# Optimization experiments

Hardware: AMD Instinct MI355X
Metric: run time of the kernel (lower is better)

Reference implementation:

```python
import jax, jax.numpy as jnp
import numpy as np

N_NODES = 50000
N_EDGES = 800000
F_IN, HID, N_CLS = 128, 64, 40
KS = 2  # kernel_size, dim=1, open B-spline, degree=1


def spline_conv(x, src, dst, pseudo, W, root, bias, num_nodes, kernel_size):
    """SplineConv (torch_geometric), dim=1, degree=1, open spline, aggr='mean'."""
    K = kernel_size
    v = pseudo[:, 0] * (K - 1)                       # map [0,1] -> [0, K-1]
    k0 = jnp.clip(jnp.floor(v), 0, K - 2)
    frac = v - k0                                    # linear (degree-1) basis
    i0 = k0.astype(jnp.int32)
    i1 = i0 + 1
    E = src.shape[0]
    e = jnp.arange(E)
    # per-edge kernel coefficients c[e,k] = sum_s basis[e,s]*[idx[e,s]==k]
    c = jnp.zeros((E, K), x.dtype).at[e, i0].add(1.0 - frac).at[e, i1].add(frac)
    xj = x[src]                                      # [E, F_in] gather
    # agg[k] = scatter-add over edges of c[e,k]*xj[e] -> [K, N, F_in]
    agg = jnp.stack([
        jax.ops.segment_sum(c[:, k:k + 1] * xj, dst, num_segments=num_nodes)
        for k in range(K)
    ])
    deg = jax.ops.segment_sum(jnp.ones((E,), x.dtype), dst, num_segments=num_nodes)
    msg = jnp.einsum('kni,kio->no', agg, W) / jnp.maximum(deg, 1.0)[:, None]
    return msg + x @ root + bias


def setup_inputs() -> dict:
    key = jax.random.key(0)
    ks = jax.random.split(key, 9)
    def glorot(k, shape):
        fan_in, fan_out = shape[-2], shape[-1]
        lim = (6.0 / (fan_in + fan_out)) ** 0.5
        return jax.random.uniform(k, shape, jnp.float32, -lim, lim)
    return {
        'x': jax.random.normal(ks[0], (N_NODES, F_IN), jnp.float32),
        'edge_index': jax.random.randint(ks[1], (2, N_EDGES), 0, N_NODES, jnp.int32),
        'edge_attr': jax.random.uniform(ks[2], (N_EDGES, 1), jnp.float32),
        'W1': glorot(ks[3], (KS, F_IN, HID)),
        'root1': glorot(ks[4], (F_IN, HID)),
        'bias1': jnp.zeros((HID,), jnp.float32),
        'W2': glorot(ks[5], (KS, HID, N_CLS)),
        'root2': glorot(ks[6], (HID, N_CLS)),
        'bias2': jnp.zeros((N_CLS,), jnp.float32),
    }


def reference(x, edge_index, edge_attr, W1, root1, bias1, W2, root2, bias2):
    src, dst = edge_index[0], edge_index[1]
    # eval mode: dropout is identity
    h = spline_conv(x, src, dst, edge_attr, W1, root1, bias1, N_NODES, KS)
    h = jax.nn.elu(h)
    out = spline_conv(h, src, dst, edge_attr, W2, root2, bias2, N_NODES, KS)
    return out
```

## Files before the change

### kernel.cpp

```cpp
#include <hip/hip_runtime.h>
#include <math.h>

#define N_NODES 50000
#define N_EDGES 800000
#define F_IN    128
#define HID     64
#define N_CLS   40

#define M1 (3 * HID)
#define M2P 128

#define RANGE_SZ 6250
#define PERM_SLICES 128
#define PERM_CHUNK (N_EDGES / PERM_SLICES)
#define EST 64

#define NW 32768
#define CW 128

using sh8 = __attribute__((ext_vector_type(8))) short;
using floatx4 = __attribute__((ext_vector_type(4))) float;

__device__ inline unsigned short f2bf(float f) {
    union { float f; unsigned int u; } c{f};
    unsigned int r = (c.u + 0x7FFF + ((c.u >> 16) & 1)) >> 16;
    return (unsigned short)r;
}
__device__ inline float bf2f(unsigned int u) {
    union { unsigned int u; float f; } c;
    c.u = u << 16;
    return c.f;
}

__global__ __launch_bounds__(256) void concat_permute(
        const float* __restrict__ W1, const float* __restrict__ root1,
        const float* __restrict__ W2, const float* __restrict__ root2,
        unsigned short* __restrict__ WT1, unsigned short* __restrict__ WT2,
        const int* __restrict__ src, const int* __restrict__ dst,
        const float* __restrict__ attr, int* __restrict__ cnt,
        unsigned int* __restrict__ edata) {
    if ((int)blockIdx.x < CW) {
        int i = blockIdx.x * 256 + threadIdx.x;
        if (i < M1 * F_IN) {
            int c = i / F_IN, k = i % F_IN;
            float val;
            if (c < HID)            val = W1[k * HID + c];
            else if (c < 2 * HID)   val = W1[F_IN * HID + k * HID + (c - HID)];
            else                    val = root1[k * HID + (c - 2 * HID)];
            WT1[i] = f2bf(val);
        } else if (i < NW) {
            int ii = i - M1 * F_IN;
            int c = ii / HID, k = ii % HID;
            float val;
            if (c < N_CLS)            val = W2[k * N_CLS + c];
            else if (c < 2 * N_CLS)   val = W2[HID * N_CLS + k * N_CLS + (c - N_CLS)];
            else if (c < 3 * N_CLS)   val = root2[k * N_CLS + (c - 2 * N_CLS)];
            else                      val = 0.0f;
            WT2[ii] = f2bf(val);
        }
    } else {
        int b2 = blockIdx.x - CW;
        int range = b2 & 7;
        int slice = b2 >> 3;
        int lo = range * RANGE_SZ;
        int e0 = slice * PERM_CHUNK;
        int e1 = e0 + PERM_CHUNK;
        for (int e = e0 + (int)threadIdx.x; e < e1; e += 256) {
            int d = dst[e];
            if ((unsigned)(d - lo) < (unsigned)RANGE_SZ) {
                int pos = atomicAdd(&cnt[d], 1);
                if (pos < EST) {
                    unsigned int q = (unsigned int)(attr[e] * 65535.0f + 0.5f);
                    edata[d * EST + pos] = (unsigned int)src[e] | (q << 16);
                }
            }
        }
    }
}

template <int KD, bool AF32, int SPLIT, int PW, int ROOTW, int MT>
__global__ __launch_bounds__(256) void gemm_mfma(const void* __restrict__ Aptr,
                                                 const unsigned short* __restrict__ Bt,
                                                 unsigned short* __restrict__ Csp,
                                                 float* __restrict__ Croot,
                                                 int Crows) {
    constexpr int KP = KD + 8;
    __shared__ unsigned short As[64 * KP];
    __shared__ unsigned short Bs[64 * KP];

    int tid = threadIdx.x;
    int row0 = blockIdx.x * 64;

    if (AF32) {
        const float* A = (const float*)Aptr;
        for (int c = tid; c < 64 * (KD / 4); c += 256) {
            int r = c / (KD / 4), q = c % (KD / 4);
            int gr = row0 + r;
            float4 v = make_float4(0.f, 0.f, 0.f, 0.f);
            if (gr < Crows) v = *(const float4*)(A + (size_t)gr * KD + q * 4);
            union { unsigned short s[4]; uint2 u; } pk;
            pk.s[0] = f2bf(v.x); pk.s[1] = f2bf(v.y);
            pk.s[2] = f2bf(v.z); pk.s[3] = f2bf(v.w);
            *(uint2*)&As[r * KP + q * 4] = pk.u;
        }
    } else {
        const unsigned short* A = (const unsigned short*)Aptr;
        for (int c = tid; c < 64 * (KD / 8); c += 256) {
            int r = c / (KD / 8), q = c % (KD / 8);
            int gr = row0 + r;
            sh8 v = {};
            if (gr < Crows) v = *(const sh8*)(A + (size_t)gr * KD + q * 8);
            *(sh8*)&As[r * KP + q * 8] = v;
        }
    }

    int wv = tid >> 6, lane = tid & 63;
    int lrow = lane & 15, lq = lane >> 4;

    for (int mt = 0; mt < MT; ++mt) {
        int c0 = mt * 64;
        __syncthreads();
        for (int c = tid; c < 64 * (KD / 8); c += 256) {
            int r = c / (KD / 8), q = c % (KD / 8);
            *(sh8*)&Bs[r * KP + q * 8] = *(const sh8*)(Bt + (size_t)(c0 + r) * KD + q * 8);
        }
        __syncthreads();

        floatx4 acc[4] = {{0.f,0.f,0.f,0.f},{0.f,0.f,0.f,0.f},{0.f,0.f,0.f,0.f},{0.f,0.f,0.f,0.f}};
#pragma unroll
        for (int kt = 0; kt < KD / 32; ++kt) {
            int kb = kt * 32 + lq * 8;
            sh8 a0 = *(const sh8*)&As[(wv * 16 + lrow) * KP + kb];
#pragma unroll
            for (int cf = 0; cf < 4; ++cf) {
                sh8 b = *(const sh8*)&Bs[(cf * 16 + lrow) * KP + kb];
                acc[cf] = __builtin_amdgcn_mfma_f32_16x16x32_bf16(a0, b, acc[cf], 0, 0, 0);
            }
        }

#pragma unroll
        for (int r = 0; r < 4; ++r) {
            int gr = row0 + wv * 16 + lq * 4 + r;
            if (gr >= Crows) continue;
#pragma unroll
            for (int cf = 0; cf < 4; ++cf) {
                int gc = c0 + cf * 16 + lrow;
                float val = acc[cf][r];
                if (gc < SPLIT) {
                    int pi = (gc < PW) ? gc * 2 : (gc - PW) * 2 + 1;
                    Csp[(size_t)gr * SPLIT + pi] = f2bf(val);
                } else if (gc < SPLIT + ROOTW) {
                    Croot[(size_t)gr * ROOTW + (gc - SPLIT)] = val;
                }
            }
        }
    }
}

__global__ __launch_bounds__(256) void gather1(const unsigned short* __restrict__ Ysp,
                                               const float* __restrict__ Yroot,
                                               const int* __restrict__ cnt,
                                               const unsigned int* __restrict__ edata,
                                               const float* __restrict__ bias1,
                                               unsigned short* __restrict__ h) {
    int wave = (blockIdx.x * blockDim.x + threadIdx.x) >> 6;
    int lane = threadIdx.x & 63;
    if (wave >= N_NODES) return;
    int deg = cnt[wave];
    deg = deg > EST ? EST : deg;
    const unsigned int* eb = edata + (size_t)wave * EST;
    const float qs = 1.0f / 65535.0f;
    float acc = 0.0f;
    if (deg <= 16) {
        unsigned int e[16], p[16];
#pragma unroll
        for (int t = 0; t < 16; ++t) e[t] = eb[t];
#pragma unroll
        for (int t = 0; t < 16; ++t) {
            int idx = (t < deg) ? (int)(e[t] & 0xffffu) : 0;
            p[t] = *(const unsigned int*)(Ysp + (size_t)idx * 128 + lane * 2);
        }
#pragma unroll
        for (int t = 0; t < 16; ++t) {
            float m = (t < deg) ? 1.0f : 0.0f;
            float v = (float)(e[t] >> 16) * qs;
            acc += m * ((1.0f - v) * bf2f(p[t] & 0xffffu) + v * bf2f(p[t] >> 16));
        }
    } else {
        unsigned int e[32], p[32];
#pragma unroll
        for (int t = 0; t < 32; ++t) e[t] = eb[t];
#pragma unroll
        for (int t = 0; t < 32; ++t) {
            int idx = (t < deg) ? (int)(e[t] & 0xffffu) : 0;
            p[t] = *(const unsigned int*)(Ysp + (size_t)idx * 128 + lane * 2);
        }
#pragma unroll
        for (int t = 0; t < 32; ++t) {
            float m = (t < deg) ? 1.0f : 0.0f;
            float v = (float)(e[t] >> 16) * qs;
            acc += m * ((1.0f - v) * bf2f(p[t] & 0xffffu) + v * bf2f(p[t] >> 16));
        }
        if (deg > 32) {
            for (int j = 32; j < deg; j += 8) {
                unsigned int e2[8], p2[8];
#pragma unroll
                for (int t = 0; t < 8; ++t) e2[t] = eb[j + t];
#pragma unroll
                for (int t = 0; t < 8; ++t) {
                    int idx = (j + t < deg) ? (int)(e2[t] & 0xffffu) : 0;
                    p2[t] = *(const unsigned int*)(Ysp + (size_t)idx * 128 + lane * 2);
                }
#pragma unroll
                for (int t = 0; t < 8; ++t) {
                    float m = (j + t < deg) ? 1.0f : 0.0f;
                    float v = (float)(e2[t] >> 16) * qs;
                    acc += m * ((1.0f - v) * bf2f(p2[t] & 0xffffu) + v * bf2f(p2[t] >> 16));
                }
            }
        }
    }
    float dg = (float)deg;
    dg = dg > 1.0f ? dg : 1.0f;
    float m = acc / dg + Yroot[(size_t)wave * HID + lane] + bias1[lane];
    m = m > 0.0f ? m : expm1f(m);
    h[(size_t)wave * HID + lane] = f2bf(m);
}

__global__ __launch_bounds__(256) void gather2(const unsigned short* __restrict__ Zsp,
                                               const float* __restrict__ Zroot,
                                               const int* __restrict__ cnt,
                                               const unsigned int* __restrict__ edata,
                                               const float* __restrict__ bias2,
                                               float* __restrict__ out) {
    int wave = (blockIdx.x * blockDim.x + threadIdx.x) >> 6;
    int lane = threadIdx.x & 63;
    if (wave >= N_NODES) return;
    if (lane >= N_CLS) return;
    int deg = cnt[wave];
    deg = deg > EST ? EST : deg;
    const unsigned int* eb = edata + (size_t)wave * EST;
    const float qs = 1.0f / 65535.0f;
    float acc = 0.0f;
    if (deg <= 16) {
        unsigned int e[16], p[16];
#pragma unroll
        for (int t = 0; t < 16; ++t) e[t] = eb[t];
#pragma unroll
        for (int t = 0; t < 16; ++t) {
            int idx = (t < deg) ? (int)(e[t] & 0xffffu) : 0;
            p[t] = *(const unsigned int*)(Zsp + (size_t)idx * 80 + lane * 2);
        }
#pragma unroll
        for (int t = 0; t < 16; ++t) {
            float m = (t < deg) ? 1.0f : 0.0f;
            float v = (float)(e[t] >> 16) * qs;
            acc += m * ((1.0f - v) * bf2f(p[t] & 0xffffu) + v * bf2f(p[t] >> 16));
        }
    } else {
        unsigned int e[32], p[32];
#pragma unroll
        for (int t = 0; t < 32; ++t) e[t] = eb[t];
#pragma unroll
        for (int t = 0; t < 32; ++t) {
            int idx = (t < deg) ? (int)(e[t] & 0xffffu) : 0;
            p[t] = *(const unsigned int*)(Zsp + (size_t)idx * 80 + lane * 2);
        }
#pragma unroll
        for (int t = 0; t < 32; ++t) {
            float m = (t < deg) ? 1.0f : 0.0f;
            float v = (float)(e[t] >> 16) * qs;
            acc += m * ((1.0f - v) * bf2f(p[t] & 0xffffu) + v * bf2f(p[t] >> 16));
        }
        if (deg > 32) {
            for (int j = 32; j < deg; j += 8) {
                unsigned int e2[8], p2[8];
#pragma unroll
                for (int t = 0; t < 8; ++t) e2[t] = eb[j + t];
#pragma unroll
                for (int t = 0; t < 8; ++t) {
                    int idx = (j + t < deg) ? (int)(e2[t] & 0xffffu) : 0;
                    p2[t] = *(const unsigned int*)(Zsp + (size_t)idx * 80 + lane * 2);
                }
#pragma unroll
                for (int t = 0; t < 8; ++t) {
                    float m = (j + t < deg) ? 1.0f : 0.0f;
                    float v = (float)(e2[t] >> 16) * qs;
                    acc += m * ((1.0f - v) * bf2f(p2[t] & 0xffffu) + v * bf2f(p2[t] >> 16));
                }
            }
        }
    }
    float dg = (float)deg;
    dg = dg > 1.0f ? dg : 1.0f;
    out[(size_t)wave * N_CLS + lane] =
        acc / dg + Zroot[(size_t)wave * N_CLS + lane] + bias2[lane];
}

extern "C" void kernel_launch(void* const* d_in, const int* in_sizes, int n_in,
                              void* d_out, int out_size, void* d_ws, size_t ws_size,
                              hipStream_t stream) {
    const float* x     = (const float*)d_in[0];
    const int*   eidx  = (const int*)d_in[1];
    const float* eattr = (const float*)d_in[2];
    const float* W1    = (const float*)d_in[3];
    const float* root1 = (const float*)d_in[4];
    const float* bias1 = (const float*)d_in[5];
    const float* W2    = (const float*)d_in[6];
    const float* root2 = (const float*)d_in[7];
    const float* bias2 = (const float*)d_in[8];
    float* out = (float*)d_out;

    const int* src = eidx;
    const int* dst = eidx + N_EDGES;

    char* base = (char*)d_ws;
    unsigned short* Ysp   = (unsigned short*)base;
    float*          Yroot = (float*)(base + 12800000);
    unsigned short* hb    = (unsigned short*)(base + 25600000);
    unsigned short* WT1   = (unsigned short*)(base + 32000000);
    unsigned short* WT2   = (unsigned short*)(base + 32049152);
    unsigned int*   edata = (unsigned int*)(base + 32065536);
    int*            cnt   = (int*)(base + 44865536);
    unsigned short* Zsp   = Ysp;
    float*          Zroot = Yroot;

    const int GB = (N_NODES + 63) / 64;

    hipMemsetAsync(cnt, 0, N_NODES * sizeof(int), stream);
    hipLaunchKernelGGL(concat_permute, dim3(CW + 8 * PERM_SLICES), dim3(256), 0, stream,
                       W1, root1, W2, root2, WT1, WT2, src, dst, eattr, cnt, edata);

    hipLaunchKernelGGL((gemm_mfma<128, true, 128, 64, 64, 3>),
                       dim3(GB), dim3(256), 0, stream,
                       (const void*)x, WT1, Ysp, Yroot, N_NODES);
    hipLaunchKernelGGL(gather1, dim3((N_NODES * 64 + 255) / 256), dim3(256), 0, stream,
                       Ysp, Yroot, cnt, edata, bias1, hb);

    hipLaunchKernelGGL((gemm_mfma<64, false, 80, 40, 40, 2>),
                       dim3(GB), dim3(256), 0, stream,
                       (const void*)hb, WT2, Zsp, Zroot, N_NODES);
    hipLaunchKernelGGL(gather2, dim3((N_NODES * 64 + 255) / 256), dim3(256), 0, stream,
                       Zsp, Zroot, cnt, edata, bias2, out);
}
```

Before: 209.1 us.

## Pin edge-bucketing work to XCDs via hardware XCC id and dynamic slice queues

Splits the old combined weight-transpose/edge-permute kernel into two kernels. The permute kernel reads the hardware XCC id and has each block work first on the node range matching its XCD, claiming edge slices through per-range atomic cursors. This keeps the cnt/edata atomics for a given destination range mostly local to one XCD's L2 and balances load dynamically. The cost is an extra kernel launch, per-slice atomic claims with two block barriers each, and reliance on the XCC-id register mapping.

```diff
diff --git a/kernel.cpp b/kernel.cpp
--- a/kernel.cpp
+++ b/kernel.cpp
@@ -16,7 +16,6 @@
 #define EST 64
 
 #define NW 32768
-#define CW 128
 
 using sh8 = __attribute__((ext_vector_type(8))) short;
 using floatx4 = __attribute__((ext_vector_type(4))) float;
@@ -32,46 +31,62 @@
     return c.f;
 }
 
-__global__ __launch_bounds__(256) void concat_permute(
-        const float* __restrict__ W1, const float* __restrict__ root1,
-        const float* __restrict__ W2, const float* __restrict__ root2,
-        unsigned short* __restrict__ WT1, unsigned short* __restrict__ WT2,
-        const int* __restrict__ src, const int* __restrict__ dst,
-        const float* __restrict__ attr, int* __restrict__ cnt,
-        unsigned int* __restrict__ edata) {
-    if ((int)blockIdx.x < CW) {
-        int i = blockIdx.x * 256 + threadIdx.x;
-        if (i < M1 * F_IN) {
-            int c = i / F_IN, k = i % F_IN;
-            float val;
-            if (c < HID)            val = W1[k * HID + c];
-            else if (c < 2 * HID)   val = W1[F_IN * HID + k * HID + (c - HID)];
-            else                    val = root1[k * HID + (c - 2 * HID)];
-            WT1[i] = f2bf(val);
-        } else if (i < NW) {
-            int ii = i - M1 * F_IN;
-            int c = ii / HID, k = ii % HID;
-            float val;
-            if (c < N_CLS)            val = W2[k * N_CLS + c];
-            else if (c < 2 * N_CLS)   val = W2[HID * N_CLS + k * N_CLS + (c - N_CLS)];
-            else if (c < 3 * N_CLS)   val = root2[k * N_CLS + (c - 2 * N_CLS)];
-            else                      val = 0.0f;
-            WT2[ii] = f2bf(val);
-        }
-    } else {
-        int b2 = blockIdx.x - CW;
-        int range = b2 & 7;
-        int slice = b2 >> 3;
+__device__ inline int get_xcc_id() {
+    int x;
+    asm volatile("s_getreg_b32 %0, hwreg(HW_REG_XCC_ID, 0, 32)" : "=s"(x));
+    return x & 7;
+}
+
+__global__ void concat_w(const float* __restrict__ W1, const float* __restrict__ root1,
+                         const float* __restrict__ W2, const float* __restrict__ root2,
+                         unsigned short* __restrict__ WT1, unsigned short* __restrict__ WT2) {
+    int i = blockIdx.x * blockDim.x + threadIdx.x;
+    if (i < M1 * F_IN) {
+        int c = i / F_IN, k = i % F_IN;
+        float val;
+        if (c < HID)            val = W1[k * HID + c];
+        else if (c < 2 * HID)   val = W1[F_IN * HID + k * HID + (c - HID)];
+        else                    val = root1[k * HID + (c - 2 * HID)];
+        WT1[i] = f2bf(val);
+    } else if (i < NW) {
+        int ii = i - M1 * F_IN;
+        int c = ii / HID, k = ii % HID;
+        float val;
+        if (c < N_CLS)            val = W2[k * N_CLS + c];
+        else if (c < 2 * N_CLS)   val = W2[HID * N_CLS + k * N_CLS + (c - N_CLS)];
+        else if (c < 3 * N_CLS)   val = root2[k * N_CLS + (c - 2 * N_CLS)];
+        else                      val = 0.0f;
+        WT2[ii] = f2bf(val);
+    }
+}
+
+__global__ __launch_bounds__(256) void permute_xcd(const int* __restrict__ src,
+                                                   const int* __restrict__ dst,
+                                                   const float* __restrict__ attr,
+                                                   int* __restrict__ cnt,
+                                                   int* __restrict__ cursor,
+                                                   unsigned int* __restrict__ edata) {
+    __shared__ int s_slice;
+    int xcd = get_xcc_id();
+    for (int k = 0; k < 8; ++k) {
+        int range = (xcd + k) & 7;
         int lo = range * RANGE_SZ;
-        int e0 = slice * PERM_CHUNK;
-        int e1 = e0 + PERM_CHUNK;
-        for (int e = e0 + (int)threadIdx.x; e < e1; e += 256) {
-            int d = dst[e];
-            if ((unsigned)(d - lo) < (unsigned)RANGE_SZ) {
-                int pos = atomicAdd(&cnt[d], 1);
-                if (pos < EST) {
-                    unsigned int q = (unsigned int)(attr[e] * 65535.0f + 0.5f);
-                    edata[d * EST + pos] = (unsigned int)src[e] | (q << 16);
+        for (;;) {
+            if (threadIdx.x == 0) s_slice = atomicAdd(&cursor[range], 1);
+            __syncthreads();
+            int slice = s_slice;
+            __syncthreads();
+            if (slice >= PERM_SLICES) break;
+            int e0 = slice * PERM_CHUNK;
+            int e1 = e0 + PERM_CHUNK;
+            for (int e = e0 + (int)threadIdx.x; e < e1; e += 256) {
+                int d = dst[e];
+                if ((unsigned)(d - lo) < (unsigned)RANGE_SZ) {
+                    int pos = atomicAdd(&cnt[d], 1);
+                    if (pos < EST) {
+                        unsigned int q = (unsigned int)(attr[e] * 65535.0f + 0.5f);
+                        edata[d * EST + pos] = (unsigned int)src[e] | (q << 16);
+                    }
                 }
             }
         }
@@ -322,14 +337,17 @@
     unsigned short* WT2   = (unsigned short*)(base + 32049152);
     unsigned int*   edata = (unsigned int*)(base + 32065536);
     int*            cnt   = (int*)(base + 44865536);
+    int*            cursor = cnt + N_NODES;
     unsigned short* Zsp   = Ysp;
     float*          Zroot = Yroot;
 
     const int GB = (N_NODES + 63) / 64;
 
-    hipMemsetAsync(cnt, 0, N_NODES * sizeof(int), stream);
-    hipLaunchKernelGGL(concat_permute, dim3(CW + 8 * PERM_SLICES), dim3(256), 0, stream,
-                       W1, root1, W2, root2, WT1, WT2, src, dst, eattr, cnt, edata);
+    hipMemsetAsync(cnt, 0, (N_NODES + 8) * sizeof(int), stream);
+    hipLaunchKernelGGL(concat_w, dim3((NW + 255) / 256), dim3(256), 0, stream,
+                       W1, root1, W2, root2, WT1, WT2);
+    hipLaunchKernelGGL(permute_xcd, dim3(1024), dim3(256), 0, stream,
+                       src, dst, eattr, cnt, cursor, edata);
 
     hipLaunchKernelGGL((gemm_mfma<128, true, 128, 64, 64, 3>),
                        dim3(GB), dim3(256), 0, stream,
```

New measurement: 310.0 us. 1.48x slower.
